# Optimization experiments

Measured on AMD Instinct MI355X. Metric: run time of the kernel, lower is better.

Reference implementation:

```python
import jax, jax.numpy as jnp
import numpy as np

B, C, H, W = 2, 3, 256, 256
K_STEPS = 50
RHO = 0.5
SIGMA_INIT = float(0.5 / np.sqrt(2.0 * C))  # sigma_init == tau_init = 0.5/sqrt(C*2)


def nabla(x):
    # forward finite differences, zero at last row/col. x: [B,C,H,W] -> [B,C,2,H,W]
    dh = jnp.pad(x[:, :, 1:, :] - x[:, :, :-1, :], ((0, 0), (0, 0), (0, 1), (0, 0)))
    dw = jnp.pad(x[:, :, :, 1:] - x[:, :, :, :-1], ((0, 0), (0, 0), (0, 0), (0, 1)))
    return jnp.stack([dh, dw], axis=2)


def nablaT(u):
    # adjoint of nabla (negative divergence). u: [B,C,2,H,W] -> [B,C,H,W]
    v0, v1 = u[:, :, 0], u[:, :, 1]
    out = jnp.zeros(v0.shape, v0.dtype)
    out = out.at[:, :, 1:, :].add(v0[:, :, :-1, :]).at[:, :, :-1, :].add(-v0[:, :, :-1, :])
    out = out.at[:, :, :, 1:].add(v1[:, :, :, :-1]).at[:, :, :, :-1].add(-v1[:, :, :, :-1])
    return out


def l12_prox_conjugate(v, lamb):
    # Moreau: prox_{sigma*(lamb*f)*}(v) = v - sigma*prox_{(lamb/sigma) f}(v/sigma)
    # which for L12 reduces to projection onto the lamb-ball per group.
    # groups: l2 over axes (1,-2,-1) = (C,H,W), one group per (B, F).
    norm = jnp.sqrt(jnp.sum(v * v, axis=(1, 3, 4), keepdims=True))
    scale = lamb / jnp.maximum(norm, lamb)  # == min(1, lamb/norm), safe at 0
    return v * scale


def l2_prox(z, y, gamma):
    # argmin_u 0.5||u-z||^2 + gamma*0.5||u-y||^2  (A = identity)
    return (z + gamma * y) / (1.0 + gamma)


def setup_inputs() -> dict:
    key = jax.random.key(0)
    y = jax.random.normal(key, (B, C, H, W), dtype=jnp.float32)
    lambd = jnp.float32(-1.0)  # learnable scalar log-regularization weight
    return {"y": y, "lambd": lambd}


def reference(y, lambd):
    elambda = jnp.exp(lambd)
    # set_init: A_dagger = identity
    x0 = y
    xt0 = jnp.zeros_like(x0)
    u0 = nabla(x0)

    def step(carry, _):
        x, xt, u, sigma, tau = carry
        u_next = l12_prox_conjugate(u + sigma * nabla(xt), elambda)
        x_next = l2_prox(x - tau * nablaT(u_next), y, tau)
        chi = 1.0 / jnp.sqrt(1.0 + 2.0 * RHO * tau)
        tau_next = tau * chi
        sigma_next = sigma / chi
        xt_next = (1.0 + chi) * x_next - chi * x
        return (x_next, xt_next, u_next, sigma_next, tau_next), None

    init = (x0, xt0, u0, jnp.float32(SIGMA_INIT), jnp.float32(SIGMA_INIT))
    (x, xt, u, _, _), _ = jax.lax.scan(step, init, None, length=K_STEPS)
    return (x, xt, u)
```

## Files before the change

### kernel.cpp

```cpp
#include <hip/hip_runtime.h>
#include <math.h>

constexpr int Cc = 3, Hh = 256;
constexpr int NX = 393216;
constexpr int R = 8;
constexpr int NBLK = 192;
constexpr int KSTEPS = 50;
constexpr int ROWQ = 128;
constexpr int BROWS = 12;
constexpr int SLOTQ = NBLK * BROWS * ROWQ;

using u64 = unsigned long long;
constexpr u64 SENT = 0x8000000080000000ull;

__device__ __forceinline__ float4 ld4(const float* p, int i) { return ((const float4*)p)[i]; }
__device__ __forceinline__ void st4(float* p, int i, float4 v) { ((float4*)p)[i] = v; }
__device__ __forceinline__ float4 mk4(float a, float b, float c, float d) { return make_float4(a, b, c, d); }
__device__ __forceinline__ u64 ldq(const u64* p) {
    return __hip_atomic_load(p, __ATOMIC_RELAXED, __HIP_MEMORY_SCOPE_AGENT);
}
__device__ __forceinline__ void stq(u64* p, u64 v) {
    __hip_atomic_store(p, v, __ATOMIC_RELAXED, __HIP_MEMORY_SCOPE_AGENT);
}
__device__ __forceinline__ void pub4(u64* w, float4 v) {
    union { float f[2]; u64 q; } a, b;
    a.f[0] = v.x; a.f[1] = v.y; b.f[0] = v.z; b.f[1] = v.w;
    stq(w, a.q); stq(w + 1, b.q);
}
__device__ __forceinline__ float4 unp(u64 lo, u64 hi) {
    union { u64 q; float f[2]; } a, b; a.q = lo; b.q = hi;
    return make_float4(a.f[0], a.f[1], b.f[0], b.f[1]);
}
__device__ __forceinline__ float4 col3(float4 P, float4 A, float4 B, float a, float b) {
    return mk4(fmaf(a, A.x, fmaf(b, B.x, P.x)), fmaf(a, A.y, fmaf(b, B.y, P.y)),
               fmaf(a, A.z, fmaf(b, B.z, P.z)), fmaf(a, A.w, fmaf(b, B.w, P.w)));
}
__device__ __forceinline__ float4 f4sub(float4 a, float4 b) {
    return mk4(a.x - b.x, a.y - b.y, a.z - b.z, a.w - b.w);
}
__device__ __forceinline__ float4 f4s(float4 a, float s) {
    return mk4(a.x * s, a.y * s, a.z * s, a.w * s);
}
__device__ __forceinline__ float4 f4fma(float s, float4 a, float4 b) {
    return mk4(fmaf(s, a.x, b.x), fmaf(s, a.y, b.y), fmaf(s, a.z, b.z), fmaf(s, a.w, b.w));
}
__device__ __forceinline__ float4 nth(float4 vm, bool up, float4 v0x, bool dn) {
    return mk4((up ? vm.x : 0.f) - (dn ? v0x.x : 0.f), (up ? vm.y : 0.f) - (dn ? v0x.y : 0.f),
               (up ? vm.z : 0.f) - (dn ? v0x.z : 0.f), (up ? vm.w : 0.f) - (dn ? v0x.w : 0.f));
}
__device__ __forceinline__ float4 ntw(float4 v1x, int c4) {
    float ul = __shfl_up(v1x.w, 1, 64);
    return mk4(((c4 > 0) ? ul : 0.f) - v1x.x, v1x.x - v1x.y, v1x.y - v1x.z,
               v1x.z - ((c4 < 63) ? v1x.w : 0.f));
}
__device__ __forceinline__ float4 gradw(float4 t, int c4) {
    float xn = __shfl_down(t.x, 1, 64);
    return mk4(t.y - t.x, t.z - t.y, t.w - t.z, (c4 < 63) ? (xn - t.w) : 0.f);
}
__device__ __forceinline__ float dot4(float4 a, float4 b) {
    return a.x * b.x + a.y * b.y + a.z * b.z + a.w * b.w;
}
__device__ __forceinline__ void barld() {
    asm volatile("s_waitcnt lgkmcnt(0)" ::: "memory");
    __builtin_amdgcn_sched_barrier(0);
    __builtin_amdgcn_s_barrier();
    __builtin_amdgcn_sched_barrier(0);
}

__global__ void init_ws(u64* h0, u64* h1, u64* h2, u64* parts) {
    int i = blockIdx.x * 256 + threadIdx.x;
    if (i < SLOTQ) { h0[i] = SENT; h1[i] = SENT; h2[i] = SENT; }
    if (i < (KSTEPS + 1) * NBLK) parts[i] = SENT;
}

__global__ void __launch_bounds__(512, 1) cp_persist(
    const float* __restrict__ y, const float* __restrict__ lambd,
    float* __restrict__ xout, float* __restrict__ xtout, float* __restrict__ uout,
    u64* __restrict__ h0, u64* __restrict__ h1, u64* __restrict__ h2,
    u64* __restrict__ parts)
{
    __shared__ float sv0[8 * 256];
    __shared__ float sxtP[9 * 256], sxtA[9 * 256], sxtB[9 * 256];
    __shared__ float2 pw[8];

    const int tid = threadIdx.x, blk = blockIdx.x;
    const int bc = blk >> 5, tile = blk & 31, r0 = tile * R;
    const int c4 = tid & 63, trow = tid >> 6;
    const int b = (bc >= Cc) ? 1 : 0;
    const float lamb = expf(lambd[0]);
    const int gh = r0 + trow;
    const int j4 = bc * 16384 + gh * 64 + c4;

    float4 yv, xcur, v0c, v1c;
    float4 xpP, xpA, xpB, p0P, p0A, p0B, p1P, p1A, p1B;
    float4 yh = mk4(0, 0, 0, 0), vmtop = yh, v0h = yh, v1h = yh, xoh = yh;
    float tau = 0.20412414523193150818f, sig = tau, chi = 0.f, sigs = 0.f;
    float g0 = 0.f, g1 = 0.f;

    auto slotp = [&](int r) -> u64* { return (r == 0) ? h0 : ((r == 1) ? h1 : h2); };
    auto wavesum2 = [&](float& a, float& bb) {
        #pragma unroll
        for (int m = 1; m < 64; m <<= 1) { a += __shfl_xor(a, m, 64); bb += __shfl_xor(bb, m, 64); }
    };

    auto pollparts = [&](int s) {
        const u64* pb = parts + (size_t)s * NBLK + b * 96;
        const int i1 = 64 + (c4 & 31);
        u64 q0, q1;
        for (;;) {
            q0 = ldq(pb + c4);
            q1 = ldq(pb + i1);
            if (__all((q0 != SENT) && (q1 != SENT))) break;
            __builtin_amdgcn_s_sleep(1);
        }
        asm volatile("" ::: "memory");
        union { u64 q; float f[2]; } a;
        a.q = q0;
        g0 = a.f[0]; g1 = a.f[1];
        a.q = q1;
        if (c4 < 32) { g0 += a.f[0]; g1 += a.f[1]; }
        wavesum2(g0, g1);
    };
    auto halopoll = [&](int sl, float al, float be) {
        u64* hbp = slotp(sl);
        if (tile > 0) {
            const u64* ra = hbp + ((size_t)(blk - 1) * BROWS) * ROWQ + 2 * c4;
            u64 a0, a1, a2, a3, a4, a5;
            for (;;) {
                a0 = ldq(ra);            a1 = ldq(ra + 1);
                a2 = ldq(ra + ROWQ);     a3 = ldq(ra + ROWQ + 1);
                a4 = ldq(ra + 2 * ROWQ); a5 = ldq(ra + 2 * ROWQ + 1);
                if (__all((a0 != SENT) && (a1 != SENT) && (a2 != SENT) &&
                          (a3 != SENT) && (a4 != SENT) && (a5 != SENT))) break;
                __builtin_amdgcn_s_sleep(1);
            }
            vmtop = col3(unp(a0, a1), unp(a2, a3), unp(a4, a5), al, be);
        } else vmtop = mk4(0, 0, 0, 0);
        if (tile < 31) {
            const u64* rb = hbp + ((size_t)(blk + 1) * BROWS) * ROWQ + 2 * c4;
            u64 b0, b1, b2, b3, b4, b5, b6, b7, b8, b9, b10, b11, b12, b13, b14, b15, b16, b17;
            for (;;) {
                b0  = ldq(rb + 3 * ROWQ);  b1  = ldq(rb + 3 * ROWQ + 1);
                b2  = ldq(rb + 4 * ROWQ);  b3  = ldq(rb + 4 * ROWQ + 1);
                b4  = ldq(rb + 5 * ROWQ);  b5  = ldq(rb + 5 * ROWQ + 1);
                b6  = ldq(rb + 6 * ROWQ);  b7  = ldq(rb + 6 * ROWQ + 1);
                b8  = ldq(rb + 7 * ROWQ);  b9  = ldq(rb + 7 * ROWQ + 1);
                b10 = ldq(rb + 8 * ROWQ);  b11 = ldq(rb + 8 * ROWQ + 1);
                b12 = ldq(rb + 9 * ROWQ);  b13 = ldq(rb + 9 * ROWQ + 1);
                b14 = ldq(rb + 10 * ROWQ); b15 = ldq(rb + 10 * ROWQ + 1);
                b16 = ldq(rb + 11 * ROWQ); b17 = ldq(rb + 11 * ROWQ + 1);
                bool ok = (b0 != SENT) && (b1 != SENT) && (b2 != SENT) && (b3 != SENT) &&
                          (b4 != SENT) && (b5 != SENT) && (b6 != SENT) && (b7 != SENT) &&
                          (b8 != SENT) && (b9 != SENT) && (b10 != SENT) && (b11 != SENT) &&
                          (b12 != SENT) && (b13 != SENT) && (b14 != SENT) && (b15 != SENT) &&
                          (b16 != SENT) && (b17 != SENT);
                if (__all(ok)) break;
                __builtin_amdgcn_s_sleep(1);
            }
            v0h = col3(unp(b0, b1),   unp(b2, b3),   unp(b4, b5),   al, be);
            v1h = col3(unp(b6, b7),   unp(b8, b9),   unp(b10, b11), al, be);
            xoh = col3(unp(b12, b13), unp(b14, b15), unp(b16, b17), al, be);
        }
        asm volatile("" ::: "memory");
    };
    auto wavenorm = [&]() {
        float pa0 = dot4(v0c, v0c), pa1 = dot4(v1c, v1c);
        wavesum2(pa0, pa1);
        if (c4 == 0) pw[trow] = make_float2(pa0, pa1);
    };
    auto pubparts = [&](int s) {
        if (tid == 0) {
            float q0 = 0.f, q1 = 0.f;
            #pragma unroll
            for (int w = 0; w < 8; ++w) { q0 += pw[w].x; q1 += pw[w].y; }
            union { float f[2]; u64 q; } pk; pk.f[0] = q0; pk.f[1] = q1;
            stq(parts + (size_t)s * NBLK + blk, pk.q);
        }
    };
    auto expand = [&](u64* hb, bool pub) {
        const float inv = 1.f / (1.f + tau), tin = tau * inv, opc = 1.f + chi;
        float4 xtP, xtA, xtB;
        {
            float4 vm = (trow > 0) ? ((float4*)(sv0 + (trow - 1) * 256))[c4] : vmtop;
            float4 NT0 = nth(vm, gh > 0, v0c, gh < Hh - 1);
            float4 NT1 = ntw(v1c, c4);
            float4 BASE = f4s(f4fma(tau, yv, xcur), inv);
            float4 xA = f4s(NT0, -tin), xB = f4s(NT1, -tin);
            xpP = BASE; xpA = xA; xpB = xB;
            xtP = f4fma(-chi, xcur, f4s(BASE, opc));
            xtA = f4s(xA, opc);
            xtB = f4s(xB, opc);
            if (trow >= 1) {
                ((float4*)(sxtP + trow * 256))[c4] = xtP;
                ((float4*)(sxtA + trow * 256))[c4] = xtA;
                ((float4*)(sxtB + trow * 256))[c4] = xtB;
            }
            if (pub && trow == 0) {
                u64* rbase = hb + ((size_t)blk * BROWS) * ROWQ;
                pub4(rbase +  9 * ROWQ + 2 * c4, BASE);
                pub4(rbase + 10 * ROWQ + 2 * c4, xA);
                pub4(rbase + 11 * ROWQ + 2 * c4, xB);
            }
        }
        if (trow == 0 && tile < 31) {
            float4 vmh = ((float4*)(sv0 + 7 * 256))[c4];
            float4 NT0h = nth(vmh, true, v0h, true);
            float4 NT1h = ntw(v1h, c4);
            float4 BASEh = f4s(f4fma(tau, yh, xoh), inv);
            ((float4*)(sxtP + 8 * 256))[c4] = f4fma(-chi, xoh, f4s(BASEh, opc));
            ((float4*)(sxtA + 8 * 256))[c4] = f4s(f4s(NT0h, -tin), opc);
            ((float4*)(sxtB + 8 * 256))[c4] = f4s(f4s(NT1h, -tin), opc);
        }
        barld();
        float4 dhP = mk4(0, 0, 0, 0), dhA = dhP, dhB = dhP;
        if (gh < Hh - 1) {
            dhP = f4sub(((float4*)(sxtP + (trow + 1) * 256))[c4], xtP);
            dhA = f4sub(((float4*)(sxtA + (trow + 1) * 256))[c4], xtA);
            dhB = f4sub(((float4*)(sxtB + (trow + 1) * 256))[c4], xtB);
        }
        float4 dwP = gradw(xtP, c4), dwA = gradw(xtA, c4), dwB = gradw(xtB, c4);
        p0P = f4s(dhP, sigs); p0A = f4fma(sigs, dhA, v0c); p0B = f4s(dhB, sigs);
        p1P = f4s(dwP, sigs); p1A = f4s(dwA, sigs); p1B = f4fma(sigs, dwB, v1c);
        if (pub) {
            u64* rbase = hb + ((size_t)blk * BROWS) * ROWQ;
            if (trow == 0) {
                pub4(rbase + 3 * ROWQ + 2 * c4, p0P);
                pub4(rbase + 4 * ROWQ + 2 * c4, p0A);
                pub4(rbase + 5 * ROWQ + 2 * c4, p0B);
                pub4(rbase + 6 * ROWQ + 2 * c4, p1P);
                pub4(rbase + 7 * ROWQ + 2 * c4, p1A);
                pub4(rbase + 8 * ROWQ + 2 * c4, p1B);
            } else if (trow == 7) {
                pub4(rbase + 0 * ROWQ + 2 * c4, p0P);
                pub4(rbase + 1 * ROWQ + 2 * c4, p0A);
                pub4(rbase + 2 * ROWQ + 2 * c4, p0B);
            }
        }
        barld();
    };

    {
        yv = ld4(y, j4);
        xcur = yv;
        v0c = (gh < Hh - 1) ? f4sub(ld4(y, j4 + 64), yv) : mk4(0, 0, 0, 0);
        v1c = gradw(yv, c4);
        ((float4*)(sv0 + trow * 256))[c4] = v0c;
        if (trow == 0) {
            if (tile < 31) {
                const int j4h = bc * 16384 + (r0 + 8) * 64 + c4;
                yh = ld4(y, j4h);
                v0h = f4sub(ld4(y, j4h + 64), yh);
                v1h = gradw(yh, c4);
                xoh = yh;
            }
            if (tile > 0) {
                float4 ym = ld4(y, bc * 16384 + (r0 - 1) * 64 + c4);
                vmtop = f4sub(yv, ym);
            }
        }
        wavenorm();
        chi = 1.f / sqrtf(1.f + tau);
        sigs = sig / chi;
        barld();
        pubparts(1);
        expand(slotp(0), true);
        pollparts(1);
        if (trow == 0) {
            float al = lamb / fmaxf(sqrtf(g0), lamb);
            float be = lamb / fmaxf(sqrtf(g1), lamb);
            halopoll(0, al, be);
        }
        tau *= chi; sig = sigs;
    }

    for (int s = 1; s < KSTEPS - 1; ++s) {
        const float al = lamb / fmaxf(sqrtf(g0), lamb);
        const float be = lamb / fmaxf(sqrtf(g1), lamb);
        chi = 1.f / sqrtf(1.f + tau);
        sigs = sig / chi;
        {
            u64* rb2 = slotp((s + 1) % 3) + ((size_t)blk * BROWS) * ROWQ;
            if (trow == 0) {
                #pragma unroll
                for (int r = 3; r < 12; ++r) {
                    stq(rb2 + r * ROWQ + 2 * c4, SENT);
                    stq(rb2 + r * ROWQ + 2 * c4 + 1, SENT);
                }
            } else if (trow == 7) {
                #pragma unroll
                for (int r = 0; r < 3; ++r) {
                    stq(rb2 + r * ROWQ + 2 * c4, SENT);
                    stq(rb2 + r * ROWQ + 2 * c4 + 1, SENT);
                }
            }
        }
        xcur = col3(xpP, xpA, xpB, al, be);
        v0c  = col3(p0P, p0A, p0B, al, be);
        v1c  = col3(p1P, p1A, p1B, al, be);
        ((float4*)(sv0 + trow * 256))[c4] = v0c;
        wavenorm();
        barld();
        pubparts(s + 1);
        expand(slotp(s % 3), true);
        pollparts(s + 1);
        if (trow == 0) {
            float al2 = lamb / fmaxf(sqrtf(g0), lamb);
            float be2 = lamb / fmaxf(sqrtf(g1), lamb);
            halopoll(s % 3, al2, be2);
        }
        tau *= chi; sig = sigs;
    }

    {
        const float al = lamb / fmaxf(sqrtf(g0), lamb);
        const float be = lamb / fmaxf(sqrtf(g1), lamb);
        chi = 1.f / sqrtf(1.f + tau);
        xcur = col3(xpP, xpA, xpB, al, be);
        v0c  = col3(p0P, p0A, p0B, al, be);
        v1c  = col3(p1P, p1A, p1B, al, be);
        ((float4*)(sv0 + trow * 256))[c4] = v0c;
        wavenorm();
        barld();
        pubparts(KSTEPS);
        const float inv = 1.f / (1.f + tau), tin = tau * inv;
        float4 vm = (trow > 0) ? ((float4*)(sv0 + (trow - 1) * 256))[c4] : vmtop;
        float4 NT0 = nth(vm, gh > 0, v0c, gh < Hh - 1);
        float4 NT1 = ntw(v1c, c4);
        float4 BASE = f4s(f4fma(tau, yv, xcur), inv);
        float4 xA = f4s(NT0, -tin), xB = f4s(NT1, -tin);
        pollparts(KSTEPS);
        const float a50 = lamb / fmaxf(sqrtf(g0), lamb);
        const float b50 = lamb / fmaxf(sqrtf(g1), lamb);
        float4 x50 = col3(BASE, xA, xB, a50, b50);
        float4 xt50 = f4fma(-chi, xcur, f4s(x50, 1.f + chi));
        const int iv4 = bc * 32768 + gh * 64 + c4;
        st4(xout, j4, x50);
        st4(xtout, j4, xt50);
        st4(uout, iv4, f4s(v0c, a50));
        st4(uout, iv4 + 16384, f4s(v1c, b50));
    }
}

extern "C" void kernel_launch(void* const* d_in, const int* in_sizes, int n_in,
                              void* d_out, int out_size, void* d_ws, size_t ws_size,
                              hipStream_t stream) {
    (void)in_sizes; (void)n_in; (void)out_size; (void)ws_size;
    const float* y     = (const float*)d_in[0];
    const float* lambd = (const float*)d_in[1];
    float* xout  = (float*)d_out;
    float* xtout = xout + NX;
    float* uout  = xout + 2 * NX;

    u64* h0 = (u64*)d_out;
    u64* h1 = h0 + SLOTQ;
    u64* h2 = (u64*)d_ws;
    u64* parts = h2 + SLOTQ;

    init_ws<<<SLOTQ / 256, 256, 0, stream>>>(h0, h1, h2, parts);
    cp_persist<<<NBLK, 512, 0, stream>>>(y, lambd, xout, xtout, uout, h0, h1, h2, parts);
}
```

Before: 216.6 us.

## Move halo polling to wave 7 and drop trailing barrier in expand

Restructures the persistent loop so the bottom-halo poll and the halo-row xt computation run in wave 7, which owns the last row, kept in registers instead of in a ninth shared-memory row. Wave 0 now only polls the top halo. This splits the halo waits across two waves and drops the trailing block barrier at the end of expand. The global-norm poll moves to the start of each iteration, and the final step reuses the loop's expand, which skips publishing on the last step. The change is meant to cut serialization and barrier costs per step, at the risk of subtle ordering bugs between shared-memory reuse and the removed barrier.

Result: faster. 189.8 us (median of 2 runs) (-12.4%).

```diff
diff --git a/kernel.cpp b/kernel.cpp
--- a/kernel.cpp
+++ b/kernel.cpp
@@ -80,7 +80,7 @@
     u64* __restrict__ parts)
 {
     __shared__ float sv0[8 * 256];
-    __shared__ float sxtP[9 * 256], sxtA[9 * 256], sxtB[9 * 256];
+    __shared__ float sxtP[8 * 256], sxtA[8 * 256], sxtB[8 * 256];
     __shared__ float2 pw[8];
 
     const int tid = threadIdx.x, blk = blockIdx.x;
@@ -94,6 +94,7 @@
     float4 yv, xcur, v0c, v1c;
     float4 xpP, xpA, xpB, p0P, p0A, p0B, p1P, p1A, p1B;
     float4 yh = mk4(0, 0, 0, 0), vmtop = yh, v0h = yh, v1h = yh, xoh = yh;
+    float4 xt8P = yh, xt8A = yh, xt8B = yh;
     float tau = 0.20412414523193150818f, sig = tau, chi = 0.f, sigs = 0.f;
     float g0 = 0.f, g1 = 0.f;
 
@@ -103,7 +104,7 @@
         for (int m = 1; m < 64; m <<= 1) { a += __shfl_xor(a, m, 64); bb += __shfl_xor(bb, m, 64); }
     };
 
-    auto pollparts = [&](int s) {
+    auto pollscale = [&](int s) {
         const u64* pb = parts + (size_t)s * NBLK + b * 96;
         const int i1 = 64 + (c4 & 31);
         u64 q0, q1;
@@ -121,9 +122,122 @@
         if (c4 < 32) { g0 += a.f[0]; g1 += a.f[1]; }
         wavesum2(g0, g1);
     };
-    auto halopoll = [&](int sl, float al, float be) {
-        u64* hbp = slotp(sl);
-        if (tile > 0) {
+    auto wavenorm = [&]() {
+        float pa0 = dot4(v0c, v0c), pa1 = dot4(v1c, v1c);
+        wavesum2(pa0, pa1);
+        if (c4 == 0) pw[trow] = make_float2(pa0, pa1);
+    };
+    auto pubparts = [&](int s) {
+        if (tid == 0) {
+            float q0 = 0.f, q1 = 0.f;
+            #pragma unroll
+            for (int w = 0; w < 8; ++w) { q0 += pw[w].x; q1 += pw[w].y; }
+            union { float f[2]; u64 q; } pk; pk.f[0] = q0; pk.f[1] = q1;
+            stq(parts + (size_t)s * NBLK + blk, pk.q);
+        }
+    };
+    auto expand = [&](u64* hb, bool pub) {
+        const float inv = 1.f / (1.f + tau), tin = tau * inv, opc = 1.f + chi;
+        float4 xtP, xtA, xtB;
+        {
+            float4 vm = (trow > 0) ? ((float4*)(sv0 + (trow - 1) * 256))[c4] : vmtop;
+            float4 NT0 = nth(vm, gh > 0, v0c, gh < Hh - 1);
+            float4 NT1 = ntw(v1c, c4);
+            float4 BASE = f4s(f4fma(tau, yv, xcur), inv);
+            float4 xA = f4s(NT0, -tin), xB = f4s(NT1, -tin);
+            xpP = BASE; xpA = xA; xpB = xB;
+            xtP = f4fma(-chi, xcur, f4s(BASE, opc));
+            xtA = f4s(xA, opc);
+            xtB = f4s(xB, opc);
+            if (trow >= 1) {
+                ((float4*)(sxtP + trow * 256))[c4] = xtP;
+                ((float4*)(sxtA + trow * 256))[c4] = xtA;
+                ((float4*)(sxtB + trow * 256))[c4] = xtB;
+            }
+            if (pub && trow == 0) {
+                u64* rbase = hb + ((size_t)blk * BROWS) * ROWQ;
+                pub4(rbase +  9 * ROWQ + 2 * c4, BASE);
+                pub4(rbase + 10 * ROWQ + 2 * c4, xA);
+                pub4(rbase + 11 * ROWQ + 2 * c4, xB);
+            }
+        }
+        if (trow == 7 && tile < 31) {
+            float4 NT0h = nth(v0c, true, v0h, true);
+            float4 NT1h = ntw(v1h, c4);
+            float4 BASEh = f4s(f4fma(tau, yh, xoh), inv);
+            xt8P = f4fma(-chi, xoh, f4s(BASEh, opc));
+            xt8A = f4s(f4s(NT0h, -tin), opc);
+            xt8B = f4s(f4s(NT1h, -tin), opc);
+        }
+        barld();
+        float4 dhP = mk4(0, 0, 0, 0), dhA = dhP, dhB = dhP;
+        if (trow < 7) {
+            dhP = f4sub(((float4*)(sxtP + (trow + 1) * 256))[c4], xtP);
+            dhA = f4sub(((float4*)(sxtA + (trow + 1) * 256))[c4], xtA);
+            dhB = f4sub(((float4*)(sxtB + (trow + 1) * 256))[c4], xtB);
+        } else if (tile < 31) {
+            dhP = f4sub(xt8P, xtP);
+            dhA = f4sub(xt8A, xtA);
+            dhB = f4sub(xt8B, xtB);
+        }
+        float4 dwP = gradw(xtP, c4), dwA = gradw(xtA, c4), dwB = gradw(xtB, c4);
+        p0P = f4s(dhP, sigs); p0A = f4fma(sigs, dhA, v0c); p0B = f4s(dhB, sigs);
+        p1P = f4s(dwP, sigs); p1A = f4s(dwA, sigs); p1B = f4fma(sigs, dwB, v1c);
+        if (pub) {
+            u64* rbase = hb + ((size_t)blk * BROWS) * ROWQ;
+            if (trow == 0) {
+                pub4(rbase + 3 * ROWQ + 2 * c4, p0P);
+                pub4(rbase + 4 * ROWQ + 2 * c4, p0A);
+                pub4(rbase + 5 * ROWQ + 2 * c4, p0B);
+                pub4(rbase + 6 * ROWQ + 2 * c4, p1P);
+                pub4(rbase + 7 * ROWQ + 2 * c4, p1A);
+                pub4(rbase + 8 * ROWQ + 2 * c4, p1B);
+            } else if (trow == 7) {
+                pub4(rbase + 0 * ROWQ + 2 * c4, p0P);
+                pub4(rbase + 1 * ROWQ + 2 * c4, p0A);
+                pub4(rbase + 2 * ROWQ + 2 * c4, p0B);
+            }
+        }
+    };
+
+    {
+        yv = ld4(y, j4);
+        xcur = yv;
+        v0c = (gh < Hh - 1) ? f4sub(ld4(y, j4 + 64), yv) : mk4(0, 0, 0, 0);
+        v1c = gradw(yv, c4);
+        ((float4*)(sv0 + trow * 256))[c4] = v0c;
+        if (trow == 7 && tile < 31) {
+            const int j4h = bc * 16384 + (r0 + 8) * 64 + c4;
+            yh = ld4(y, j4h);
+            v0h = f4sub(ld4(y, j4h + 64), yh);
+            v1h = gradw(yh, c4);
+            xoh = yh;
+        }
+        if (trow == 0 && tile > 0) {
+            float4 ym = ld4(y, bc * 16384 + (r0 - 1) * 64 + c4);
+            vmtop = f4sub(yv, ym);
+        }
+        wavenorm();
+        chi = 1.f / sqrtf(1.f + tau);
+        sigs = sig / chi;
+        barld();
+        pubparts(1);
+        expand(slotp(0), true);
+        tau *= chi; sig = sigs;
+    }
+
+    for (int s = 1; s < KSTEPS; ++s) {
+        pollscale(s);
+        const float al = lamb / fmaxf(sqrtf(g0), lamb);
+        const float be = lamb / fmaxf(sqrtf(g1), lamb);
+        chi = 1.f / sqrtf(1.f + tau);
+        sigs = sig / chi;
+        xcur = col3(xpP, xpA, xpB, al, be);
+        v0c  = col3(p0P, p0A, p0B, al, be);
+        v1c  = col3(p1P, p1A, p1B, al, be);
+        ((float4*)(sv0 + trow * 256))[c4] = v0c;
+        u64* hbp = slotp((s - 1) % 3);
+        if (trow == 0 && tile > 0) {
             const u64* ra = hbp + ((size_t)(blk - 1) * BROWS) * ROWQ + 2 * c4;
             u64 a0, a1, a2, a3, a4, a5;
             for (;;) {
@@ -135,8 +249,10 @@
                 __builtin_amdgcn_s_sleep(1);
             }
             vmtop = col3(unp(a0, a1), unp(a2, a3), unp(a4, a5), al, be);
-        } else vmtop = mk4(0, 0, 0, 0);
-        if (tile < 31) {
+        } else if (trow == 0) {
+            vmtop = mk4(0, 0, 0, 0);
+        }
+        if (trow == 7 && tile < 31) {
             const u64* rb = hbp + ((size_t)(blk + 1) * BROWS) * ROWQ + 2 * c4;
             u64 b0, b1, b2, b3, b4, b5, b6, b7, b8, b9, b10, b11, b12, b13, b14, b15, b16, b17;
             for (;;) {
@@ -162,122 +278,6 @@
             xoh = col3(unp(b12, b13), unp(b14, b15), unp(b16, b17), al, be);
         }
         asm volatile("" ::: "memory");
-    };
-    auto wavenorm = [&]() {
-        float pa0 = dot4(v0c, v0c), pa1 = dot4(v1c, v1c);
-        wavesum2(pa0, pa1);
-        if (c4 == 0) pw[trow] = make_float2(pa0, pa1);
-    };
-    auto pubparts = [&](int s) {
-        if (tid == 0) {
-            float q0 = 0.f, q1 = 0.f;
-            #pragma unroll
-            for (int w = 0; w < 8; ++w) { q0 += pw[w].x; q1 += pw[w].y; }
-            union { float f[2]; u64 q; } pk; pk.f[0] = q0; pk.f[1] = q1;
-            stq(parts + (size_t)s * NBLK + blk, pk.q);
-        }
-    };
-    auto expand = [&](u64* hb, bool pub) {
-        const float inv = 1.f / (1.f + tau), tin = tau * inv, opc = 1.f + chi;
-        float4 xtP, xtA, xtB;
-        {
-            float4 vm = (trow > 0) ? ((float4*)(sv0 + (trow - 1) * 256))[c4] : vmtop;
-            float4 NT0 = nth(vm, gh > 0, v0c, gh < Hh - 1);
-            float4 NT1 = ntw(v1c, c4);
-            float4 BASE = f4s(f4fma(tau, yv, xcur), inv);
-            float4 xA = f4s(NT0, -tin), xB = f4s(NT1, -tin);
-            xpP = BASE; xpA = xA; xpB = xB;
-            xtP = f4fma(-chi, xcur, f4s(BASE, opc));
-            xtA = f4s(xA, opc);
-            xtB = f4s(xB, opc);
-            if (trow >= 1) {
-                ((float4*)(sxtP + trow * 256))[c4] = xtP;
-                ((float4*)(sxtA + trow * 256))[c4] = xtA;
-                ((float4*)(sxtB + trow * 256))[c4] = xtB;
-            }
-            if (pub && trow == 0) {
-                u64* rbase = hb + ((size_t)blk * BROWS) * ROWQ;
-                pub4(rbase +  9 * ROWQ + 2 * c4, BASE);
-                pub4(rbase + 10 * ROWQ + 2 * c4, xA);
-                pub4(rbase + 11 * ROWQ + 2 * c4, xB);
-            }
-        }
-        if (trow == 0 && tile < 31) {
-            float4 vmh = ((float4*)(sv0 + 7 * 256))[c4];
-            float4 NT0h = nth(vmh, true, v0h, true);
-            float4 NT1h = ntw(v1h, c4);
-            float4 BASEh = f4s(f4fma(tau, yh, xoh), inv);
-            ((float4*)(sxtP + 8 * 256))[c4] = f4fma(-chi, xoh, f4s(BASEh, opc));
-            ((float4*)(sxtA + 8 * 256))[c4] = f4s(f4s(NT0h, -tin), opc);
-            ((float4*)(sxtB + 8 * 256))[c4] = f4s(f4s(NT1h, -tin), opc);
-        }
-        barld();
-        float4 dhP = mk4(0, 0, 0, 0), dhA = dhP, dhB = dhP;
-        if (gh < Hh - 1) {
-            dhP = f4sub(((float4*)(sxtP + (trow + 1) * 256))[c4], xtP);
-            dhA = f4sub(((float4*)(sxtA + (trow + 1) * 256))[c4], xtA);
-            dhB = f4sub(((float4*)(sxtB + (trow + 1) * 256))[c4], xtB);
-        }
-        float4 dwP = gradw(xtP, c4), dwA = gradw(xtA, c4), dwB = gradw(xtB, c4);
-        p0P = f4s(dhP, sigs); p0A = f4fma(sigs, dhA, v0c); p0B = f4s(dhB, sigs);
-        p1P = f4s(dwP, sigs); p1A = f4s(dwA, sigs); p1B = f4fma(sigs, dwB, v1c);
-        if (pub) {
-            u64* rbase = hb + ((size_t)blk * BROWS) * ROWQ;
-            if (trow == 0) {
-                pub4(rbase + 3 * ROWQ + 2 * c4, p0P);
-                pub4(rbase + 4 * ROWQ + 2 * c4, p0A);
-                pub4(rbase + 5 * ROWQ + 2 * c4, p0B);
-                pub4(rbase + 6 * ROWQ + 2 * c4, p1P);
-                pub4(rbase + 7 * ROWQ + 2 * c4, p1A);
-                pub4(rbase + 8 * ROWQ + 2 * c4, p1B);
-            } else if (trow == 7) {
-                pub4(rbase + 0 * ROWQ + 2 * c4, p0P);
-                pub4(rbase + 1 * ROWQ + 2 * c4, p0A);
-                pub4(rbase + 2 * ROWQ + 2 * c4, p0B);
-            }
-        }
-        barld();
-    };
-
-    {
-        yv = ld4(y, j4);
-        xcur = yv;
-        v0c = (gh < Hh - 1) ? f4sub(ld4(y, j4 + 64), yv) : mk4(0, 0, 0, 0);
-        v1c = gradw(yv, c4);
-        ((float4*)(sv0 + trow * 256))[c4] = v0c;
-        if (trow == 0) {
-            if (tile < 31) {
-                const int j4h = bc * 16384 + (r0 + 8) * 64 + c4;
-                yh = ld4(y, j4h);
-                v0h = f4sub(ld4(y, j4h + 64), yh);
-                v1h = gradw(yh, c4);
-                xoh = yh;
-            }
-            if (tile > 0) {
-                float4 ym = ld4(y, bc * 16384 + (r0 - 1) * 64 + c4);
-                vmtop = f4sub(yv, ym);
-            }
-        }
-        wavenorm();
-        chi = 1.f / sqrtf(1.f + tau);
-        sigs = sig / chi;
-        barld();
-        pubparts(1);
-        expand(slotp(0), true);
-        pollparts(1);
-        if (trow == 0) {
-            float al = lamb / fmaxf(sqrtf(g0), lamb);
-            float be = lamb / fmaxf(sqrtf(g1), lamb);
-            halopoll(0, al, be);
-        }
-        tau *= chi; sig = sigs;
-    }
-
-    for (int s = 1; s < KSTEPS - 1; ++s) {
-        const float al = lamb / fmaxf(sqrtf(g0), lamb);
-        const float be = lamb / fmaxf(sqrtf(g1), lamb);
-        chi = 1.f / sqrtf(1.f + tau);
-        sigs = sig / chi;
         {
             u64* rb2 = slotp((s + 1) % 3) + ((size_t)blk * BROWS) * ROWQ;
             if (trow == 0) {
@@ -294,44 +294,18 @@
                 }
             }
         }
-        xcur = col3(xpP, xpA, xpB, al, be);
-        v0c  = col3(p0P, p0A, p0B, al, be);
-        v1c  = col3(p1P, p1A, p1B, al, be);
-        ((float4*)(sv0 + trow * 256))[c4] = v0c;
         wavenorm();
         barld();
         pubparts(s + 1);
-        expand(slotp(s % 3), true);
-        pollparts(s + 1);
-        if (trow == 0) {
-            float al2 = lamb / fmaxf(sqrtf(g0), lamb);
-            float be2 = lamb / fmaxf(sqrtf(g1), lamb);
-            halopoll(s % 3, al2, be2);
-        }
+        expand(slotp(s % 3), s < KSTEPS - 1);
         tau *= chi; sig = sigs;
     }
 
     {
-        const float al = lamb / fmaxf(sqrtf(g0), lamb);
-        const float be = lamb / fmaxf(sqrtf(g1), lamb);
-        chi = 1.f / sqrtf(1.f + tau);
-        xcur = col3(xpP, xpA, xpB, al, be);
-        v0c  = col3(p0P, p0A, p0B, al, be);
-        v1c  = col3(p1P, p1A, p1B, al, be);
-        ((float4*)(sv0 + trow * 256))[c4] = v0c;
-        wavenorm();
-        barld();
-        pubparts(KSTEPS);
-        const float inv = 1.f / (1.f + tau), tin = tau * inv;
-        float4 vm = (trow > 0) ? ((float4*)(sv0 + (trow - 1) * 256))[c4] : vmtop;
-        float4 NT0 = nth(vm, gh > 0, v0c, gh < Hh - 1);
-        float4 NT1 = ntw(v1c, c4);
-        float4 BASE = f4s(f4fma(tau, yv, xcur), inv);
-        float4 xA = f4s(NT0, -tin), xB = f4s(NT1, -tin);
-        pollparts(KSTEPS);
+        pollscale(KSTEPS);
         const float a50 = lamb / fmaxf(sqrtf(g0), lamb);
         const float b50 = lamb / fmaxf(sqrtf(g1), lamb);
-        float4 x50 = col3(BASE, xA, xB, a50, b50);
+        float4 x50 = col3(xpP, xpA, xpB, a50, b50);
         float4 xt50 = f4fma(-chi, xcur, f4s(x50, 1.f + chi));
         const int iv4 = bc * 32768 + gh * 64 + c4;
         st4(xout, j4, x50);
```
